# Kernel optimization log

Measured on AMD Instinct MI355X. Metric: run time of the kernel, lower is better.

## Reference

```python
import jax, jax.numpy as jnp
import numpy as np

N = 20000        # nodes per type
E = 320000       # edges per type (avg degree 16)
H = 8            # heads
F0 = 128         # initial feature dim
F_UNI = 256      # n_unified
F_OUT = 64       # n_units per layer
N_USER = 20000   # shape_ret[0]
N_CLASSES = 2


def setup_inputs() -> dict:
    key = jax.random.key(0)
    ks = jax.random.split(key, 32)
    nrm = lambda k, s: jax.random.normal(k, s, dtype=jnp.float32) * 0.05
    inp = {
        "hemb0": nrm(ks[0], (N, F0)),
        "hemb1": nrm(ks[1], (N, F0)),
        "W0": nrm(ks[2], (F0, F_UNI)),
        "W1": nrm(ks[3], (F0, F_UNI)),
    }
    i = 4
    for t in range(2):
        for l, fin in enumerate([F_UNI, H * F_OUT]):
            inp[f"g{t}l{l}_w"] = nrm(ks[i], (H, fin, F_OUT)); i += 1
            inp[f"g{t}l{l}_asrc"] = nrm(ks[i], (H, F_OUT)); i += 1
            inp[f"g{t}l{l}_atrg"] = nrm(ks[i], (H, F_OUT)); i += 1
    inp["aw1"] = nrm(ks[i], (F_UNI, F_OUT)); i += 1
    inp["aw2"] = nrm(ks[i], (F_OUT, F_OUT)); i += 1
    inp["am"] = nrm(ks[i], (F_OUT,)); i += 1
    inp["fc_w"] = nrm(ks[i], (F_OUT * 3, N_CLASSES)); i += 1
    inp["fc_b"] = jnp.zeros((N_CLASSES,), jnp.float32); i += 1
    inp["edge0"] = jax.random.randint(ks[i], (2, E), 0, N, dtype=jnp.int32); i += 1
    inp["edge1"] = jax.random.randint(ks[i], (2, E), 0, N, dtype=jnp.int32)
    return inp


def spgat(h, src, trg, w, asrc, atrg):
    """Sparse GAT layer: h [N,f_in], edge list src/trg [E] -> [N,H,f_out]."""
    n = h.shape[0]
    hp = jnp.einsum('nf,hfo->hno', h, w)              # [H,N,O]
    s = jnp.einsum('hno,ho->nh', hp, asrc)            # [N,H]
    t = jnp.einsum('hno,ho->nh', hp, atrg)            # [N,H]
    e = jax.nn.leaky_relu(s[src] + t[trg], negative_slope=0.2)  # [E,H]
    ex = jnp.exp(e - jnp.max(e))                      # global max shift (as in source)
    denom = jax.ops.segment_sum(ex, trg, num_segments=n)[trg] + 1e-16
    alpha = ex / denom                                # [E,H]
    msg = jnp.transpose(hp, (1, 0, 2))[src] * alpha[:, :, None]  # [E,H,O]
    return jax.ops.segment_sum(msg, trg, num_segments=n)         # [N,H,O]


def reference(hemb0, hemb1, W0, W1,
              g0l0_w, g0l0_asrc, g0l0_atrg, g0l1_w, g0l1_asrc, g0l1_atrg,
              g1l0_w, g1l0_asrc, g1l0_atrg, g1l1_w, g1l1_asrc, g1l1_atrg,
              aw1, aw2, am, fc_w, fc_b, edge0, edge1):
    trans0 = hemb0 @ W0                                # [N,F_UNI]
    trans1 = hemb1 @ W1
    stacks = [
        (trans0, edge0, (g0l0_w, g0l0_asrc, g0l0_atrg), (g0l1_w, g0l1_asrc, g0l1_atrg)),
        (trans1, edge1, (g1l0_w, g1l0_asrc, g1l0_atrg), (g1l1_w, g1l1_asrc, g1l1_atrg)),
    ]
    heter = []
    for trans, edge, p0, p1 in stacks:
        src, trg = edge[0], edge[1]
        x = spgat(trans, src, trg, *p0)                # [N,H,F_OUT]
        x = jax.nn.elu(x.reshape(N, -1))               # [N,H*F_OUT]
        x = spgat(x, src, trg, *p1).mean(axis=1)       # [N,F_OUT]
        heter.append(x[:N_USER][:, None, :])
    type_aware = jnp.concatenate(heter, axis=1)        # [N_USER, 2, F_OUT]
    # faithful to source: feature = trans_emb[0] where trans_emb is the LAST
    # type's transformed embedding -> row 0, shape [F_UNI], broadcast over nodes
    feature = trans1[0]
    q = jnp.tanh(feature @ aw1 + type_aware @ aw2)     # [N_USER,2,F_OUT]
    beta = jax.nn.softmax(q @ am, axis=-1)             # [N_USER,2]
    fusion = jnp.einsum('nr,nrd->nd', beta, type_aware)[:, None, :]
    ret = jnp.concatenate([type_aware, fusion], axis=1).reshape(N_USER, -1)
    return jax.nn.log_softmax(ret @ fc_w + fc_b, axis=-1)   # [N_USER, 2]
```

## Files before the change

### kernel.cpp

```cpp
#include <hip/hip_runtime.h>
#include <hip/hip_bf16.h>


typedef __hip_bfloat16 bf16;
typedef __attribute__((ext_vector_type(8))) short short8;
typedef __attribute__((ext_vector_type(4))) float f32x4;

__device__ __forceinline__ float bf2f(bf16 v) { return __bfloat162float(v); }
__device__ __forceinline__ float ldin(const void* p, long i, int f32) {
  return f32 ? ((const float*)p)[i] : bf2f(((const bf16*)p)[i]);
}
__device__ __forceinline__ short f2bfbits(float f) {
  bf16 h = __float2bfloat16(f);
  return *reinterpret_cast<short*>(&h);
}
__device__ __forceinline__ float bfbits2f(short b) {
  unsigned u = ((unsigned)(unsigned short)b) << 16;
  return __uint_as_float(u);
}

__global__ __launch_bounds__(64) void detect_kernel(const void* __restrict__ x,
                                                    int* __restrict__ flag) {
  int tid = threadIdx.x;
  float m = 0.f;
  for (int i = tid; i < 2048; i += 64) {
    float v = fabsf(bf2f(((const bf16*)x)[i]));
    if (!(v <= 1e3f)) v = 1e9f;
    m = fmaxf(m, v);
  }
#pragma unroll
  for (int off = 32; off; off >>= 1) m = fmaxf(m, __shfl_xor(m, off));
  if (tid == 0) flag[0] = (m > 1e3f) ? 1 : 0;
}

#define GBM 128
#define GBN 64
#define GBK 64

__device__ __forceinline__ int swz(int row, int kbyte) {
  return row * 128 + (kbyte ^ ((row & 7) << 4));
}

__global__ __launch_bounds__(256) void gemm_mfma(const void* __restrict__ A, int amode,
                                                 const void* __restrict__ B, int bmode,
                                                 bf16* __restrict__ C,
                                                 int M, int K, int Nc,
                                                 const void* __restrict__ stasrc,
                                                 const void* __restrict__ statrg,
                                                 float* __restrict__ svp,
                                                 float* __restrict__ tvp,
                                                 const int* __restrict__ flag) {
  __shared__ bf16 As[GBM * GBK];
  __shared__ bf16 Bs[GBN * GBK];
  const int f32 = flag[0];
  const int af32 = (amode == 1) ? f32 : 0;
  const int m0 = blockIdx.x * GBM;
  const int n0 = blockIdx.y * GBN;
  const int tid = threadIdx.x;
  const int lane = tid & 63;
  const int wrow = (tid >> 6) * 32;

  f32x4 acc[2][4];
#pragma unroll
  for (int m = 0; m < 2; m++)
#pragma unroll
    for (int n = 0; n < 4; n++)
#pragma unroll
      for (int r = 0; r < 4; r++) acc[m][n][r] = 0.f;

  for (int kt = 0; kt < K; kt += GBK) {
#pragma unroll
    for (int j = 0; j < 4; j++) {
      int idx = tid + j * 256;
      int row = idx >> 3;
      int ks = idx & 7;
      int gm = m0 + row;
      short8 v;
#pragma unroll
      for (int e = 0; e < 8; e++) v[e] = 0;
      if (gm < M) {
        long base = (long)gm * K + kt + ks * 8;
        if (!af32) {
          v = *(const short8*)((const bf16*)A + base);
        } else {
          const float* Af = (const float*)A + base;
#pragma unroll
          for (int e = 0; e < 8; e++) v[e] = f2bfbits(Af[e]);
        }
      }
      *(short8*)((char*)As + swz(row, ks * 16)) = v;
    }
    {
      int n = tid & 63;
      int ks0 = tid >> 6;
#pragma unroll
      for (int jj = 0; jj < 2; jj++) {
        int ks = ks0 + jj * 4;
        int k = kt + ks * 8;
        int col = n0 + n;
        long base;
        int cstr;
        if (bmode == 0) { base = (long)k * Nc + col; cstr = Nc; }
        else { base = ((long)(col >> 6) * K + k) * 64 + (col & 63); cstr = 64; }
        short8 v;
        if (f32) {
          const float* Bf = (const float*)B;
#pragma unroll
          for (int e = 0; e < 8; e++) v[e] = f2bfbits(Bf[base + (long)e * cstr]);
        } else {
          const bf16* Bh = (const bf16*)B;
#pragma unroll
          for (int e = 0; e < 8; e++) v[e] = *(const short*)&Bh[base + (long)e * cstr];
        }
        *(short8*)((char*)Bs + swz(n, ks * 16)) = v;
      }
    }
    __syncthreads();
#pragma unroll
    for (int kh = 0; kh < 2; kh++) {
      int klane = kh * 64 + ((lane >> 4) << 4);
      short8 af[2], bfr[4];
#pragma unroll
      for (int m = 0; m < 2; m++) {
        int row = wrow + m * 16 + (lane & 15);
        af[m] = *(const short8*)((const char*)As + swz(row, klane));
      }
#pragma unroll
      for (int n = 0; n < 4; n++) {
        int col = n * 16 + (lane & 15);
        bfr[n] = *(const short8*)((const char*)Bs + swz(col, klane));
      }
#pragma unroll
      for (int m = 0; m < 2; m++)
#pragma unroll
        for (int n = 0; n < 4; n++)
          acc[m][n] = __builtin_amdgcn_mfma_f32_16x16x32_bf16(af[m], bfr[n], acc[m][n], 0, 0, 0);
    }
    __syncthreads();
  }
  if (svp) {
    const int h = blockIdx.y;
    const int cl = lane & 15;
    float av[4], bv[4];
#pragma unroll
    for (int n = 0; n < 4; n++) {
      av[n] = ldin(stasrc, h * 64 + n * 16 + cl, f32);
      bv[n] = ldin(statrg, h * 64 + n * 16 + cl, f32);
    }
#pragma unroll
    for (int m = 0; m < 2; m++) {
#pragma unroll
      for (int r = 0; r < 4; r++) {
        float s = 0.f, t = 0.f;
#pragma unroll
        for (int n = 0; n < 4; n++) {
          s += acc[m][n][r] * av[n];
          t += acc[m][n][r] * bv[n];
        }
#pragma unroll
        for (int off = 1; off <= 8; off <<= 1) {
          s += __shfl_xor(s, off);
          t += __shfl_xor(t, off);
        }
        int row = m0 + wrow + m * 16 + ((lane >> 4) << 2) + r;
        if (cl == 0 && row < M) {
          svp[(long)row * 8 + h] = s;
          tvp[(long)row * 8 + h] = t;
        }
      }
    }
  }
#pragma unroll
  for (int m = 0; m < 2; m++) {
#pragma unroll
    for (int r = 0; r < 4; r++) {
      int row = m0 + wrow + m * 16 + ((lane >> 4) << 2) + r;
      if (row < M) {
#pragma unroll
        for (int n = 0; n < 4; n++) {
          int col = n0 + n * 16 + (lane & 15);
          C[(long)row * Nc + col] = __float2bfloat16(acc[m][n][r]);
        }
      }
    }
  }
}

__global__ void hist2_kernel(const int* __restrict__ trg0, const int* __restrict__ trg1,
                             int* __restrict__ deg, int E, int N) {
  int e = blockIdx.x * 256 + threadIdx.x;
  if (e < E) atomicAdd(&deg[trg0[e]], 1);
  else if (e < 2 * E) atomicAdd(&deg[N + trg1[e - E]], 1);
}

__global__ __launch_bounds__(1024) void scan_kernel(const int* __restrict__ degb,
                                                    int* __restrict__ rpb,
                                                    int* __restrict__ filb, int N) {
  const int* deg = degb + (long)blockIdx.x * N;
  int* row_ptr = rpb + (long)blockIdx.x * (N + 1);
  int* fil = filb + (long)blockIdx.x * N;
  __shared__ int sums[1024];
  int tid = threadIdx.x;
  int chunk = (N + 1023) >> 10;
  int start = tid * chunk;
  int end = start + chunk;
  if (start > N) start = N;
  if (end > N) end = N;
  int s = 0;
  for (int i = start; i < end; i++) s += deg[i];
  sums[tid] = s;
  __syncthreads();
  for (int off = 1; off < 1024; off <<= 1) {
    int add = (tid >= off) ? sums[tid - off] : 0;
    __syncthreads();
    sums[tid] += add;
    __syncthreads();
  }
  int run = (tid > 0) ? sums[tid - 1] : 0;
  for (int i = start; i < end; i++) {
    row_ptr[i] = run;
    fil[i] = run;
    run += deg[i];
  }
  if (tid == 0) row_ptr[N] = sums[1023];
}

__global__ void fill2_kernel(const int* __restrict__ src0, const int* __restrict__ trg0,
                             const int* __restrict__ src1, const int* __restrict__ trg1,
                             int* __restrict__ filb, int* __restrict__ colb, int E, int N) {
  int e = blockIdx.x * 256 + threadIdx.x;
  if (e < E) {
    int t = trg0[e];
    int pos = atomicAdd(&filb[t], 1);
    colb[pos] = src0[e];
  } else if (e < 2 * E) {
    int ee = e - E;
    int t = trg1[ee];
    int pos = atomicAdd(&filb[N + t], 1);
    colb[E + pos] = src1[ee];
  }
}

__device__ __forceinline__ float exleaky(float v) {
  v = v > 0.f ? v : 0.2f * v;
  return __expf(v);
}

__global__ __launch_bounds__(256) void aggregate(const bf16* __restrict__ hp,
                                                 const float* __restrict__ sv,
                                                 const float* __restrict__ tv,
                                                 const int* __restrict__ row_ptr,
                                                 const int* __restrict__ col_src,
                                                 void* __restrict__ out, int N, int mode) {
  __shared__ float s_acc[2][512];
  __shared__ float s_den[2][64];
  const int wid = threadIdx.x >> 6;
  const int lane = threadIdx.x & 63;
  const int slot = wid >> 1;
  const int half = wid & 1;
  const int n = blockIdx.x * 2 + slot;
  const int act = (n < N);
  int start = 0, deg = 0;
  if (act) {
    start = row_ptr[n];
    deg = row_ptr[n + 1] - start;
  }
  const int h = lane >> 3;
  const float tvh = act ? tv[(long)n * 8 + h] : 0.f;
  const bf16* __restrict__ hpc = hp + lane * 8;

  float acc[8] = {0.f, 0.f, 0.f, 0.f, 0.f, 0.f, 0.f, 0.f};
  float den = 0.f;

#define AG_LOAD(EB, V0, V1, V2, V3, Q0, Q1, Q2, Q3)                 \
  {                                                                 \
    int t0 = __shfl(mysrc, (EB) + 0), t1 = __shfl(mysrc, (EB) + 1); \
    int t2 = __shfl(mysrc, (EB) + 2), t3 = __shfl(mysrc, (EB) + 3); \
    V0 = *(const short8*)(hpc + (long)t0 * 512);                    \
    V1 = *(const short8*)(hpc + (long)t1 * 512);                    \
    V2 = *(const short8*)(hpc + (long)t2 * 512);                    \
    V3 = *(const short8*)(hpc + (long)t3 * 512);                    \
    Q0 = sv[(long)t0 * 8 + h];                                      \
    Q1 = sv[(long)t1 * 8 + h];                                      \
    Q2 = sv[(long)t2 * 8 + h];                                      \
    Q3 = sv[(long)t3 * 8 + h];                                      \
  }
#define AG_ACC(V0, V1, V2, V3, Q0, Q1, Q2, Q3)                      \
  {                                                                 \
    float a0 = exleaky(Q0 + tvh), a1 = exleaky(Q1 + tvh);           \
    float a2 = exleaky(Q2 + tvh), a3 = exleaky(Q3 + tvh);           \
    den += a0 + a1 + a2 + a3;                                       \
    _Pragma("unroll")                                               \
    for (int j = 0; j < 8; j++)                                     \
      acc[j] += a0 * bfbits2f(V0[j]) + a1 * bfbits2f(V1[j]) +       \
                a2 * bfbits2f(V2[j]) + a3 * bfbits2f(V3[j]);        \
  }

  for (int base = 0; base < deg; base += 64) {
    int cnt = deg - base;
    if (cnt > 64) cnt = 64;
    int mysrc = (lane < cnt) ? col_src[start + base + lane] : 0;
    int ngrp = cnt >> 2;
    int g = half;
    if (g < ngrp) {
      short8 v0, v1, v2, v3;
      float q0, q1, q2, q3;
      AG_LOAD(g * 4, v0, v1, v2, v3, q0, q1, q2, q3);
      for (int g2 = g + 2; g2 < ngrp; g2 += 2) {
        short8 w0 = v0, w1 = v1, w2 = v2, w3 = v3;
        float p0 = q0, p1 = q1, p2 = q2, p3 = q3;
        AG_LOAD(g2 * 4, v0, v1, v2, v3, q0, q1, q2, q3);
        AG_ACC(w0, w1, w2, w3, p0, p1, p2, p3);
      }
      AG_ACC(v0, v1, v2, v3, q0, q1, q2, q3);
    }
    if (half == 0) {
      for (int e = ngrp * 4; e < cnt; e++) {
        int s0 = __shfl(mysrc, e);
        short8 v = *(const short8*)(hpc + (long)s0 * 512);
        float a = exleaky(sv[(long)s0 * 8 + h] + tvh);
        den += a;
#pragma unroll
        for (int j = 0; j < 8; j++) acc[j] += a * bfbits2f(v[j]);
      }
    }
  }

  if (half == 1) {
#pragma unroll
    for (int j = 0; j < 8; j++) s_acc[slot][j * 64 + lane] = acc[j];
    s_den[slot][lane] = den;
  }
  __syncthreads();
  if (half == 0 && act) {
    den += s_den[slot][lane] + 1e-16f;
#pragma unroll
    for (int j = 0; j < 8; j++) acc[j] += s_acc[slot][j * 64 + lane];
    const float dinv = 1.f / den;
    if (mode == 0) {
      short8 o8;
#pragma unroll
      for (int j = 0; j < 8; j++) {
        float s = acc[j] * dinv;
        float ev = s > 0.f ? s : expm1f(s);
        o8[j] = f2bfbits(ev);
      }
      *(short8*)((bf16*)out + (long)n * 512 + lane * 8) = o8;
    } else {
      float r[8];
#pragma unroll
      for (int j = 0; j < 8; j++) r[j] = acc[j] * dinv;
#pragma unroll
      for (int m = 8; m <= 32; m <<= 1)
#pragma unroll
        for (int j = 0; j < 8; j++) r[j] += __shfl_xor(r[j], m);
      if (lane < 8) {
        float* o = (float*)out + (long)n * 128 + lane * 8;
#pragma unroll
        for (int j = 0; j < 8; j++) o[j] = r[j] * 0.125f;
      }
    }
  }
}

__global__ __launch_bounds__(256) void favec_kernel(const bf16* __restrict__ trans1,
                                                    const void* __restrict__ aw1,
                                                    float* __restrict__ favec,
                                                    const int* __restrict__ flag) {
  const int f32 = flag[0];
  __shared__ float part[4][64];
  const int o = threadIdx.x & 63;
  const int wv = threadIdx.x >> 6;
  float acc = 0.f;
#pragma unroll
  for (int kk = 0; kk < 64; kk++) {
    int k = wv * 64 + kk;
    acc += bf2f(trans1[k]) * ldin(aw1, (long)k * 64 + o, f32);
  }
  part[wv][o] = acc;
  __syncthreads();
  if (threadIdx.x < 64) favec[o] = part[0][o] + part[1][o] + part[2][o] + part[3][o];
}

#define FN 16
__global__ __launch_bounds__(256) void final_kernel(const float* __restrict__ ta,
                                                    const float* __restrict__ favec,
                                                    const void* __restrict__ aw2,
                                                    const void* __restrict__ am,
                                                    const void* __restrict__ fcw,
                                                    const void* __restrict__ fcb,
                                                    void* __restrict__ out, int N,
                                                    const int* __restrict__ flag) {
  const int f32 = flag[0];
  __shared__ float s_w[64 * 64];
  __shared__ float s_fc[384];
  __shared__ float s_misc[130];
  __shared__ float s_ta[FN * 128];
  const int tid = threadIdx.x;
  const int n0 = blockIdx.x * FN;
  for (int i = tid; i < 4096; i += 256) s_w[i] = ldin(aw2, i, f32);
  for (int i = tid; i < 384; i += 256) s_fc[i] = ldin(fcw, i, f32);
  if (tid < 64) s_misc[tid] = favec[tid];
  else if (tid < 128) s_misc[tid] = ldin(am, tid - 64, f32);
  else if (tid < 130) s_misc[tid] = ldin(fcb, tid - 128, f32);
  for (int idx = tid; idx < FN * 128; idx += 256) {
    int ni = idx >> 7;
    int j = idx & 127;
    int k = j >> 1, r = j & 1;
    int n = n0 + ni;
    s_ta[idx] = (n < N) ? ta[(long)n * 128 + r * 64 + k] : 0.f;
  }
  __syncthreads();
  const int o = tid & 63;
  const int wv = tid >> 6;
#pragma unroll
  for (int ni4 = 0; ni4 < 4; ni4++) {
    const int ni = wv * 4 + ni4;
    const int n = n0 + ni;
    if (n >= N) continue;
    const float* tb = &s_ta[ni * 128];
    float acc0 = s_misc[o], acc1 = acc0;
#pragma unroll 8
    for (int k = 0; k < 64; k++) {
      float2 t2 = *(const float2*)(tb + k * 2);
      float w = s_w[k * 64 + o];
      acc0 += t2.x * w;
      acc1 += t2.y * w;
    }
    float ta0 = tb[o * 2];
    float ta1 = tb[o * 2 + 1];
    float amv = s_misc[64 + o];
    float p0 = tanhf(acc0) * amv;
    float p1 = tanhf(acc1) * amv;
#pragma unroll
    for (int off = 32; off > 0; off >>= 1) {
      p0 += __shfl_xor(p0, off);
      p1 += __shfl_xor(p1, off);
    }
    float mx = fmaxf(p0, p1);
    float e0 = __expf(p0 - mx), e1 = __expf(p1 - mx);
    float b0 = e0 / (e0 + e1), b1 = e1 / (e0 + e1);
    float fus = b0 * ta0 + b1 * ta1;
    float l0 = ta0 * s_fc[o * 2 + 0] + ta1 * s_fc[(64 + o) * 2 + 0] + fus * s_fc[(128 + o) * 2 + 0];
    float l1 = ta0 * s_fc[o * 2 + 1] + ta1 * s_fc[(64 + o) * 2 + 1] + fus * s_fc[(128 + o) * 2 + 1];
#pragma unroll
    for (int off = 32; off > 0; off >>= 1) {
      l0 += __shfl_xor(l0, off);
      l1 += __shfl_xor(l1, off);
    }
    if (o == 0) {
      l0 += s_misc[128];
      l1 += s_misc[129];
      float m2 = fmaxf(l0, l1);
      float lse = m2 + logf(__expf(l0 - m2) + __expf(l1 - m2));
      if (f32) {
        ((float*)out)[n * 2 + 0] = l0 - lse;
        ((float*)out)[n * 2 + 1] = l1 - lse;
      } else {
        ((bf16*)out)[n * 2 + 0] = __float2bfloat16(l0 - lse);
        ((bf16*)out)[n * 2 + 1] = __float2bfloat16(l1 - lse);
      }
    }
  }
}

extern "C" void kernel_launch(void* const* d_in, const int* in_sizes, int n_in,
                              void* d_out, int out_size, void* d_ws, size_t ws_size,
                              hipStream_t stream) {
  constexpr int N = 20000, E = 320000, H = 8, F0 = 128, FU = 256, FO = 64;
  const void* hemb[2] = {d_in[0], d_in[1]};
  const void* W[2] = {d_in[2], d_in[3]};
  const void* gw[2][2] = {{d_in[4], d_in[7]}, {d_in[10], d_in[13]}};
  const void* gasrc[2][2] = {{d_in[5], d_in[8]}, {d_in[11], d_in[14]}};
  const void* gatrg[2][2] = {{d_in[6], d_in[9]}, {d_in[12], d_in[15]}};
  const void* aw1 = d_in[16];
  const void* aw2 = d_in[17];
  const void* am = d_in[18];
  const void* fcw = d_in[19];
  const void* fcb = d_in[20];
  const int* edge[2] = {(const int*)d_in[21], (const int*)d_in[22]};

  char* p = (char*)d_ws;
  auto alloc = [&](size_t bytes) -> void* {
    void* r = (void*)p;
    p += (bytes + 255) & ~(size_t)255;
    return r;
  };
  int* flag = (int*)alloc(4);
  bf16* trans = (bf16*)alloc((size_t)N * FU * 2);
  bf16* hp = (bf16*)alloc((size_t)N * H * FO * 2);
  bf16* xbuf = (bf16*)alloc((size_t)N * H * FO * 2);
  float* sv = (float*)alloc((size_t)N * H * 4);
  float* tv = (float*)alloc((size_t)N * H * 4);
  float* ta = (float*)alloc((size_t)N * 2 * FO * 4);
  float* favec = (float*)alloc(FO * 4);
  int* degb = (int*)alloc((size_t)2 * N * 4);
  int* rpb = (int*)alloc((size_t)2 * (N + 1) * 4);
  int* filb = (int*)alloc((size_t)2 * N * 4);
  int* colb = (int*)alloc((size_t)2 * E * 4);

  detect_kernel<<<1, 64, 0, stream>>>(hemb[0], flag);

  hipMemsetAsync(degb, 0, (size_t)2 * N * 4, stream);
  hist2_kernel<<<(2 * E + 255) / 256, 256, 0, stream>>>(edge[0] + E, edge[1] + E, degb, E, N);
  scan_kernel<<<2, 1024, 0, stream>>>(degb, rpb, filb, N);
  fill2_kernel<<<(2 * E + 255) / 256, 256, 0, stream>>>(edge[0], edge[0] + E,
                                                        edge[1], edge[1] + E, filb, colb, E, N);

  const int gmx = (N + GBM - 1) / GBM;
  const int gagg = (N + 1) / 2;

  for (int t = 0; t < 2; t++) {
    const int* rp = rpb + (size_t)t * (N + 1);
    const int* col = colb + (size_t)t * E;
    gemm_mfma<<<dim3(gmx, FU / GBN), 256, 0, stream>>>(hemb[t], 1, W[t], 0, trans,
                                                       N, F0, FU,
                                                       nullptr, nullptr, nullptr, nullptr, flag);
    gemm_mfma<<<dim3(gmx, (H * FO) / GBN), 256, 0, stream>>>(trans, 0, gw[t][0], 1, hp,
                                                             N, FU, H * FO,
                                                             gasrc[t][0], gatrg[t][0], sv, tv, flag);
    aggregate<<<gagg, 256, 0, stream>>>(hp, sv, tv, rp, col, xbuf, N, 0);
    gemm_mfma<<<dim3(gmx, (H * FO) / GBN), 256, 0, stream>>>(xbuf, 0, gw[t][1], 1, hp,
                                                             N, H * FO, H * FO,
                                                             gasrc[t][1], gatrg[t][1], sv, tv, flag);
    aggregate<<<gagg, 256, 0, stream>>>(hp, sv, tv, rp, col, ta + t * FO, N, 1);
  }

  favec_kernel<<<1, 256, 0, stream>>>(trans, aw1, favec, flag);
  final_kernel<<<(N + FN - 1) / FN, 256, 0, stream>>>(ta, favec, aw2, am, fcw, fcb, d_out, N, flag);
}
```

Measured before the change: 571.4 us.

## Batch both node-type GAT stacks into single launches and use one wave per node

Passes the two edge types' GEMM and aggregation work through struct arguments indexed by blockIdx.z/y, so each stage is one launch covering both types when the workspace is large enough. The aggregate kernel now assigns one full wave per destination node, four nodes per block, replacing the two-wave split that merged partials through shared memory and a block barrier. This is meant to cut launch count, fill the GPU better with larger grids, and remove the LDS reduction and sync. In exchange it doubles intermediate buffer memory and each wave walks its node's whole edge list alone.

```diff
diff --git a/kernel.cpp b/kernel.cpp
--- a/kernel.cpp
+++ b/kernel.cpp
@@ -18,6 +18,25 @@
   unsigned u = ((unsigned)(unsigned short)b) << 16;
   return __uint_as_float(u);
 }
+
+struct GArg {
+  const void* A[2];
+  const void* B[2];
+  bf16* C[2];
+  const void* sa[2];
+  const void* sb[2];
+  float* sv[2];
+  float* tv[2];
+};
+
+struct AArg {
+  const bf16* hp[2];
+  const float* sv[2];
+  const float* tv[2];
+  const int* rp[2];
+  const int* col[2];
+  void* out[2];
+};
 
 __global__ __launch_bounds__(64) void detect_kernel(const void* __restrict__ x,
                                                     int* __restrict__ flag) {
@@ -41,17 +60,19 @@
   return row * 128 + (kbyte ^ ((row & 7) << 4));
 }
 
-__global__ __launch_bounds__(256) void gemm_mfma(const void* __restrict__ A, int amode,
-                                                 const void* __restrict__ B, int bmode,
-                                                 bf16* __restrict__ C,
+__global__ __launch_bounds__(256) void gemm_mfma(GArg g, int amode, int bmode,
                                                  int M, int K, int Nc,
-                                                 const void* __restrict__ stasrc,
-                                                 const void* __restrict__ statrg,
-                                                 float* __restrict__ svp,
-                                                 float* __restrict__ tvp,
                                                  const int* __restrict__ flag) {
   __shared__ bf16 As[GBM * GBK];
   __shared__ bf16 Bs[GBN * GBK];
+  const int z = blockIdx.z;
+  const void* __restrict__ A = g.A[z];
+  const void* __restrict__ B = g.B[z];
+  bf16* __restrict__ C = g.C[z];
+  const void* stasrc = g.sa[z];
+  const void* statrg = g.sb[z];
+  float* svp = g.sv[z];
+  float* tvp = g.tv[z];
   const int f32 = flag[0];
   const int af32 = (amode == 1) ? f32 : 0;
   const int m0 = blockIdx.x * GBM;
@@ -246,31 +267,26 @@
   return __expf(v);
 }
 
-__global__ __launch_bounds__(256) void aggregate(const bf16* __restrict__ hp,
-                                                 const float* __restrict__ sv,
-                                                 const float* __restrict__ tv,
-                                                 const int* __restrict__ row_ptr,
-                                                 const int* __restrict__ col_src,
-                                                 void* __restrict__ out, int N, int mode) {
-  __shared__ float s_acc[2][512];
-  __shared__ float s_den[2][64];
+__global__ __launch_bounds__(256) void aggregate(AArg aa, int N, int mode) {
+  const int ty = blockIdx.y;
+  const bf16* __restrict__ hpb = aa.hp[ty];
+  const float* __restrict__ svb = aa.sv[ty];
+  const float* __restrict__ tvb = aa.tv[ty];
+  const int* __restrict__ rp = aa.rp[ty];
+  const int* __restrict__ colv = aa.col[ty];
+  void* __restrict__ outp = aa.out[ty];
   const int wid = threadIdx.x >> 6;
   const int lane = threadIdx.x & 63;
-  const int slot = wid >> 1;
-  const int half = wid & 1;
-  const int n = blockIdx.x * 2 + slot;
-  const int act = (n < N);
-  int start = 0, deg = 0;
-  if (act) {
-    start = row_ptr[n];
-    deg = row_ptr[n + 1] - start;
-  }
+  const int n = blockIdx.x * 4 + wid;
+  if (n >= N) return;
+  const int start = rp[n];
+  const int deg = rp[n + 1] - start;
   const int h = lane >> 3;
-  const float tvh = act ? tv[(long)n * 8 + h] : 0.f;
-  const bf16* __restrict__ hpc = hp + lane * 8;
+  const float tvh = tvb[(long)n * 8 + h];
+  const bf16* __restrict__ hpc = hpb + lane * 8;
 
   float acc[8] = {0.f, 0.f, 0.f, 0.f, 0.f, 0.f, 0.f, 0.f};
-  float den = 0.f;
+  float den = 1e-16f;
 
 #define AG_LOAD(EB, V0, V1, V2, V3, Q0, Q1, Q2, Q3)                 \
   {                                                                 \
@@ -280,10 +296,10 @@
     V1 = *(const short8*)(hpc + (long)t1 * 512);                    \
     V2 = *(const short8*)(hpc + (long)t2 * 512);                    \
     V3 = *(const short8*)(hpc + (long)t3 * 512);                    \
-    Q0 = sv[(long)t0 * 8 + h];                                      \
-    Q1 = sv[(long)t1 * 8 + h];                                      \
-    Q2 = sv[(long)t2 * 8 + h];                                      \
-    Q3 = sv[(long)t3 * 8 + h];                                      \
+    Q0 = svb[(long)t0 * 8 + h];                                     \
+    Q1 = svb[(long)t1 * 8 + h];                                     \
+    Q2 = svb[(long)t2 * 8 + h];                                     \
+    Q3 = svb[(long)t3 * 8 + h];                                     \
   }
 #define AG_ACC(V0, V1, V2, V3, Q0, Q1, Q2, Q3)                      \
   {                                                                 \
@@ -299,66 +315,52 @@
   for (int base = 0; base < deg; base += 64) {
     int cnt = deg - base;
     if (cnt > 64) cnt = 64;
-    int mysrc = (lane < cnt) ? col_src[start + base + lane] : 0;
-    int ngrp = cnt >> 2;
-    int g = half;
-    if (g < ngrp) {
+    int mysrc = (lane < cnt) ? colv[start + base + lane] : 0;
+    int nfull = cnt & ~3;
+    if (nfull) {
       short8 v0, v1, v2, v3;
       float q0, q1, q2, q3;
-      AG_LOAD(g * 4, v0, v1, v2, v3, q0, q1, q2, q3);
-      for (int g2 = g + 2; g2 < ngrp; g2 += 2) {
+      AG_LOAD(0, v0, v1, v2, v3, q0, q1, q2, q3);
+      for (int e = 4; e < nfull; e += 4) {
         short8 w0 = v0, w1 = v1, w2 = v2, w3 = v3;
         float p0 = q0, p1 = q1, p2 = q2, p3 = q3;
-        AG_LOAD(g2 * 4, v0, v1, v2, v3, q0, q1, q2, q3);
+        AG_LOAD(e, v0, v1, v2, v3, q0, q1, q2, q3);
         AG_ACC(w0, w1, w2, w3, p0, p1, p2, p3);
       }
       AG_ACC(v0, v1, v2, v3, q0, q1, q2, q3);
     }
-    if (half == 0) {
-      for (int e = ngrp * 4; e < cnt; e++) {
-        int s0 = __shfl(mysrc, e);
-        short8 v = *(const short8*)(hpc + (long)s0 * 512);
-        float a = exleaky(sv[(long)s0 * 8 + h] + tvh);
-        den += a;
-#pragma unroll
-        for (int j = 0; j < 8; j++) acc[j] += a * bfbits2f(v[j]);
-      }
-    }
-  }
-
-  if (half == 1) {
-#pragma unroll
-    for (int j = 0; j < 8; j++) s_acc[slot][j * 64 + lane] = acc[j];
-    s_den[slot][lane] = den;
-  }
-  __syncthreads();
-  if (half == 0 && act) {
-    den += s_den[slot][lane] + 1e-16f;
-#pragma unroll
-    for (int j = 0; j < 8; j++) acc[j] += s_acc[slot][j * 64 + lane];
-    const float dinv = 1.f / den;
-    if (mode == 0) {
-      short8 o8;
-#pragma unroll
-      for (int j = 0; j < 8; j++) {
-        float s = acc[j] * dinv;
-        float ev = s > 0.f ? s : expm1f(s);
-        o8[j] = f2bfbits(ev);
-      }
-      *(short8*)((bf16*)out + (long)n * 512 + lane * 8) = o8;
-    } else {
-      float r[8];
-#pragma unroll
-      for (int j = 0; j < 8; j++) r[j] = acc[j] * dinv;
-#pragma unroll
-      for (int m = 8; m <= 32; m <<= 1)
-#pragma unroll
-        for (int j = 0; j < 8; j++) r[j] += __shfl_xor(r[j], m);
-      if (lane < 8) {
-        float* o = (float*)out + (long)n * 128 + lane * 8;
-#pragma unroll
-        for (int j = 0; j < 8; j++) o[j] = r[j] * 0.125f;
-      }
+    for (int e = nfull; e < cnt; e++) {
+      int s0 = __shfl(mysrc, e);
+      short8 v = *(const short8*)(hpc + (long)s0 * 512);
+      float a = exleaky(svb[(long)s0 * 8 + h] + tvh);
+      den += a;
+#pragma unroll
+      for (int j = 0; j < 8; j++) acc[j] += a * bfbits2f(v[j]);
+    }
+  }
+
+  const float dinv = 1.f / den;
+  if (mode == 0) {
+    short8 o8;
+#pragma unroll
+    for (int j = 0; j < 8; j++) {
+      float s = acc[j] * dinv;
+      float ev = s > 0.f ? s : expm1f(s);
+      o8[j] = f2bfbits(ev);
+    }
+    *(short8*)((bf16*)outp + (long)n * 512 + lane * 8) = o8;
+  } else {
+    float r[8];
+#pragma unroll
+    for (int j = 0; j < 8; j++) r[j] = acc[j] * dinv;
+#pragma unroll
+    for (int m = 8; m <= 32; m <<= 1)
+#pragma unroll
+      for (int j = 0; j < 8; j++) r[j] += __shfl_xor(r[j], m);
+    if (lane < 8) {
+      float* o = (float*)outp + (long)n * 128 + lane * 8;
+#pragma unroll
+      for (int j = 0; j < 8; j++) o[j] = r[j] * 0.125f;
     }
   }
 }
@@ -480,6 +482,20 @@
   const void* fcb = d_in[20];
   const int* edge[2] = {(const int*)d_in[21], (const int*)d_in[22]};
 
+  const size_t szTrans = (size_t)N * FU * 2;
+  const size_t szHp = (size_t)N * 512 * 2;
+  const size_t szSv = (size_t)N * 8 * 4;
+  size_t need = 0;
+  auto addsz = [&](size_t b) { need += (b + 255) & ~(size_t)255; };
+  addsz(4);
+  addsz(szTrans * 2); addsz(szHp * 2); addsz(szHp * 2);
+  addsz(szSv * 2); addsz(szSv * 2);
+  addsz((size_t)N * 128 * 4); addsz(256);
+  addsz((size_t)2 * N * 4); addsz((size_t)2 * (N + 1) * 4);
+  addsz((size_t)2 * N * 4); addsz((size_t)2 * E * 4);
+  const bool batched = (ws_size >= need + 4096);
+  const int TB = batched ? 2 : 1;
+
   char* p = (char*)d_ws;
   auto alloc = [&](size_t bytes) -> void* {
     void* r = (void*)p;
@@ -487,13 +503,13 @@
     return r;
   };
   int* flag = (int*)alloc(4);
-  bf16* trans = (bf16*)alloc((size_t)N * FU * 2);
-  bf16* hp = (bf16*)alloc((size_t)N * H * FO * 2);
-  bf16* xbuf = (bf16*)alloc((size_t)N * H * FO * 2);
-  float* sv = (float*)alloc((size_t)N * H * 4);
-  float* tv = (float*)alloc((size_t)N * H * 4);
-  float* ta = (float*)alloc((size_t)N * 2 * FO * 4);
-  float* favec = (float*)alloc(FO * 4);
+  bf16* trans = (bf16*)alloc(szTrans * TB);
+  bf16* hp = (bf16*)alloc(szHp * TB);
+  bf16* xbuf = (bf16*)alloc(szHp * TB);
+  float* sv = (float*)alloc(szSv * TB);
+  float* tv = (float*)alloc(szSv * TB);
+  float* ta = (float*)alloc((size_t)N * 128 * 4);
+  float* favec = (float*)alloc(256);
   int* degb = (int*)alloc((size_t)2 * N * 4);
   int* rpb = (int*)alloc((size_t)2 * (N + 1) * 4);
   int* filb = (int*)alloc((size_t)2 * N * 4);
@@ -508,24 +524,63 @@
                                                         edge[1], edge[1] + E, filb, colb, E, N);
 
   const int gmx = (N + GBM - 1) / GBM;
-  const int gagg = (N + 1) / 2;
-
-  for (int t = 0; t < 2; t++) {
-    const int* rp = rpb + (size_t)t * (N + 1);
-    const int* col = colb + (size_t)t * E;
-    gemm_mfma<<<dim3(gmx, FU / GBN), 256, 0, stream>>>(hemb[t], 1, W[t], 0, trans,
-                                                       N, F0, FU,
-                                                       nullptr, nullptr, nullptr, nullptr, flag);
-    gemm_mfma<<<dim3(gmx, (H * FO) / GBN), 256, 0, stream>>>(trans, 0, gw[t][0], 1, hp,
-                                                             N, FU, H * FO,
-                                                             gasrc[t][0], gatrg[t][0], sv, tv, flag);
-    aggregate<<<gagg, 256, 0, stream>>>(hp, sv, tv, rp, col, xbuf, N, 0);
-    gemm_mfma<<<dim3(gmx, (H * FO) / GBN), 256, 0, stream>>>(xbuf, 0, gw[t][1], 1, hp,
-                                                             N, H * FO, H * FO,
-                                                             gasrc[t][1], gatrg[t][1], sv, tv, flag);
-    aggregate<<<gagg, 256, 0, stream>>>(hp, sv, tv, rp, col, ta + t * FO, N, 1);
-  }
-
-  favec_kernel<<<1, 256, 0, stream>>>(trans, aw1, favec, flag);
+  const int npass = batched ? 1 : 2;
+  const int TC = batched ? 2 : 1;
+
+  auto transP = [&](int b) { return trans + (size_t)b * N * FU; };
+  auto hpP = [&](int b) { return hp + (size_t)b * N * 512; };
+  auto xbufP = [&](int b) { return xbuf + (size_t)b * N * 512; };
+  auto svP = [&](int b) { return sv + (size_t)b * N * 8; };
+  auto tvP = [&](int b) { return tv + (size_t)b * N * 8; };
+
+  for (int pass = 0; pass < npass; pass++) {
+    int types[2] = {batched ? 0 : pass, batched ? 1 : pass};
+    int bufs[2] = {batched ? 0 : 0, batched ? 1 : 0};
+
+    GArg g0{};
+    for (int i = 0; i < TC; i++) {
+      int t = types[i], b = bufs[i];
+      g0.A[i] = hemb[t]; g0.B[i] = W[t]; g0.C[i] = transP(b);
+      g0.sa[i] = nullptr; g0.sb[i] = nullptr; g0.sv[i] = nullptr; g0.tv[i] = nullptr;
+    }
+    gemm_mfma<<<dim3(gmx, FU / GBN, TC), 256, 0, stream>>>(g0, 1, 0, N, F0, FU, flag);
+
+    GArg g1{};
+    for (int i = 0; i < TC; i++) {
+      int t = types[i], b = bufs[i];
+      g1.A[i] = transP(b); g1.B[i] = gw[t][0]; g1.C[i] = hpP(b);
+      g1.sa[i] = gasrc[t][0]; g1.sb[i] = gatrg[t][0]; g1.sv[i] = svP(b); g1.tv[i] = tvP(b);
+    }
+    gemm_mfma<<<dim3(gmx, (H * FO) / GBN, TC), 256, 0, stream>>>(g1, 0, 1, N, FU, H * FO, flag);
+
+    AArg a0{};
+    for (int i = 0; i < TC; i++) {
+      int t = types[i], b = bufs[i];
+      a0.hp[i] = hpP(b); a0.sv[i] = svP(b); a0.tv[i] = tvP(b);
+      a0.rp[i] = rpb + (size_t)t * (N + 1); a0.col[i] = colb + (size_t)t * E;
+      a0.out[i] = xbufP(b);
+    }
+    aggregate<<<dim3((N + 3) / 4, TC), 256, 0, stream>>>(a0, N, 0);
+
+    GArg g2{};
+    for (int i = 0; i < TC; i++) {
+      int t = types[i], b = bufs[i];
+      g2.A[i] = xbufP(b); g2.B[i] = gw[t][1]; g2.C[i] = hpP(b);
+      g2.sa[i] = gasrc[t][1]; g2.sb[i] = gatrg[t][1]; g2.sv[i] = svP(b); g2.tv[i] = tvP(b);
+    }
+    gemm_mfma<<<dim3(gmx, (H * FO) / GBN, TC), 256, 0, stream>>>(g2, 0, 1, N, H * FO, H * FO, flag);
+
+    AArg a1{};
+    for (int i = 0; i < TC; i++) {
+      int t = types[i], b = bufs[i];
+      a1.hp[i] = hpP(b); a1.sv[i] = svP(b); a1.tv[i] = tvP(b);
+      a1.rp[i] = rpb + (size_t)t * (N + 1); a1.col[i] = colb + (size_t)t * E;
+      a1.out[i] = ta + (size_t)t * FO;
+    }
+    aggregate<<<dim3((N + 3) / 4, TC), 256, 0, stream>>>(a1, N, 1);
+  }
+
+  const bf16* trans1 = batched ? transP(1) : transP(0);
+  favec_kernel<<<1, 256, 0, stream>>>(trans1, aw1, favec, flag);
   final_kernel<<<(N + FN - 1) / FN, 256, 0, stream>>>(ta, favec, aw2, am, fcw, fcb, d_out, N, flag);
 }
```

Result: faster. 542.6 us (-5.0%).
